# Kernel tuning notes

Hardware: AMD Instinct MI355X
Metric: run time of the kernel (lower is better)

Reference implementation:

```python
import jax, jax.numpy as jnp
import numpy as np

N = 50000      # nodes
E = 640000     # edges
F_IN = 128
F_OUT = 128


def setup_inputs() -> dict:
    key = jax.random.key(0)
    k1, k2, k3, k4, k5 = jax.random.split(key, 5)
    x = jax.random.normal(k1, (N, F_IN), jnp.float32)
    # binary observation mask (torch: mask.float())
    mask = (jax.random.uniform(k2, (N, F_IN)) < 0.5).astype(jnp.float32)
    edge_index = jax.random.randint(k3, (2, E), 0, N, dtype=jnp.int32)
    W = jax.random.normal(k4, (F_OUT, F_IN), jnp.float32) / np.sqrt(F_IN)
    b = jax.random.normal(k5, (F_OUT,), jnp.float32) * 0.01
    return {"x": x, "mask": mask, "edge_index": edge_index, "W": W, "b": b}


def reference(x, mask, edge_index, W, b):
    row, col = edge_index[0], edge_index[1]

    # --- get_symmetrically_normalized_adjacency: DAD = D^-1/2 A D^-1/2 ---
    ones_e = jnp.ones((edge_index.shape[1],), x.dtype)
    deg = jax.ops.segment_sum(ones_e, col, num_segments=N)
    dinv = jnp.where(deg > 0, deg ** -0.5, 0.0)  # inf -> 0
    w = dinv[row] * dinv[col]                    # [E] normalized edge weights

    def spmm(m):  # (adj @ m)[i] = sum_{e: row_e=i} w_e * m[col_e]
        return jax.ops.segment_sum(w[:, None] * m[col], row, num_segments=N)

    # x[x.isnan()] = 0
    x = jnp.nan_to_num(x)

    # adj @ ones_like(x) == rowsum(adj) broadcast over features
    rowsum = jax.ops.segment_sum(w, row, num_segments=N)  # [N]
    numerator = rowsum[:, None] * spmm(mask * x)          # [N, F_IN]
    denominator = spmm(mask)                              # [N, F_IN]
    ratio = jnp.nan_to_num(numerator / denominator)

    return ratio @ W.T + b
```

## Files before the change

kernel.cpp:

```cpp
#include <hip/hip_runtime.h>
#include <math.h>

#define NN 50000
#define NE 640000
#define F  128
#define NB 196
#define PACKB 12500
#define CHB 256
#define ECHUNK 2500
#define WPAD 136

typedef __attribute__((ext_vector_type(8))) short short8;
typedef __attribute__((ext_vector_type(4))) float floatx4;

__device__ inline unsigned f2bf_pk(float f0, float f1) {
    unsigned u0 = __float_as_uint(f0), u1 = __float_as_uint(f1);
    u0 = (u0 + 0x7fffu + ((u0 >> 16) & 1u)) >> 16;
    u1 = (u1 + 0x7fffu + ((u1 >> 16) & 1u)) >> 16;
    return (u1 << 16) | u0;
}

__device__ inline unsigned ilv4(unsigned a, unsigned b) {
    a = (a | (a << 2)) & 0x33u; a = (a | (a << 1)) & 0x55u;
    b = (b | (b << 2)) & 0x33u; b = (b | (b << 1)) & 0x55u;
    return a | (b << 1);
}

__global__ __launch_bounds__(256) void pc_kernel(const float* __restrict__ x,
                                                 const float* __restrict__ mask,
                                                 const int* __restrict__ row,
                                                 const int* __restrict__ col,
                                                 unsigned* __restrict__ mx,
                                                 unsigned char* __restrict__ rec,
                                                 int* __restrict__ crow,
                                                 int* __restrict__ ccol) {
    if (blockIdx.x < PACKB) {
        int lane = threadIdx.x & 63;
        int n = blockIdx.x * 4 + (threadIdx.x >> 6);
        float2 xv = ((const float2*)x)[(size_t)n * 64 + lane];
        float2 mv = ((const float2*)mask)[(size_t)n * 64 + lane];
        float x0 = (xv.x != xv.x) ? 0.f : xv.x;
        float x1 = (xv.y != xv.y) ? 0.f : xv.y;
        float p0 = (mv.x != 0.f) ? x0 : 0.f;
        float p1 = (mv.y != 0.f) ? x1 : 0.f;
        mx[(size_t)n * 64 + lane] = f2bf_pk(p0, p1);
        unsigned long long b0 = __ballot(mv.x != 0.f);
        unsigned long long b1 = __ballot(mv.y != 0.f);
        if (lane < 16) {
            unsigned nib0 = (unsigned)(b0 >> (4 * lane)) & 0xFu;
            unsigned nib1 = (unsigned)(b1 >> (4 * lane)) & 0xFu;
            rec[(size_t)n * 32 + lane] = (unsigned char)ilv4(nib0, nib1);
        }
    } else {
        __shared__ int hr[NB], hc[NB];
        for (int i = threadIdx.x; i < NB; i += 256) { hr[i] = 0; hc[i] = 0; }
        __syncthreads();
        int bid = blockIdx.x - PACKB;
        int e0 = bid * ECHUNK, e1 = e0 + ECHUNK;
        for (int e = e0 + threadIdx.x; e < e1; e += 256) {
            atomicAdd(&hr[row[e] >> 8], 1);
            atomicAdd(&hc[col[e] >> 8], 1);
        }
        __syncthreads();
        for (int i = threadIdx.x; i < NB; i += 256) {
            atomicAdd(&crow[i], hr[i]);
            atomicAdd(&ccol[i], hc[i]);
        }
    }
}

__global__ __launch_bounds__(256) void cscan_kernel(const int* __restrict__ crow,
                                                    const int* __restrict__ ccol,
                                                    int* __restrict__ crow_base,
                                                    int* __restrict__ ccol_base,
                                                    int* __restrict__ crow_cur,
                                                    int* __restrict__ ccol_cur,
                                                    int* __restrict__ rowstart) {
    __shared__ int ws[4];
    int t = threadIdx.x, lane = t & 63, wid = t >> 6;
    {
        int v = (t < NB) ? crow[t] : 0;
        int incl = v;
        #pragma unroll
        for (int off = 1; off < 64; off <<= 1) { int s = __shfl_up(incl, off); if (lane >= off) incl += s; }
        if (lane == 63) ws[wid] = incl;
        __syncthreads();
        int wbase = 0;
        for (int k = 0; k < wid; k++) wbase += ws[k];
        int ex = wbase + incl - v;
        if (t < NB) { crow_base[t] = ex; crow_cur[t] = ex; }
        if (t == 0) { crow_base[NB] = NE; rowstart[NN] = NE; }
        __syncthreads();
    }
    {
        int v = (t < NB) ? ccol[t] : 0;
        int incl = v;
        #pragma unroll
        for (int off = 1; off < 64; off <<= 1) { int s = __shfl_up(incl, off); if (lane >= off) incl += s; }
        if (lane == 63) ws[wid] = incl;
        __syncthreads();
        int wbase = 0;
        for (int k = 0; k < wid; k++) wbase += ws[k];
        int ex = wbase + incl - v;
        if (t < NB) { ccol_base[t] = ex; ccol_cur[t] = ex; }
        if (t == 0) ccol_base[NB] = NE;
    }
}

__global__ __launch_bounds__(256) void scatter_kernel(const int* __restrict__ row,
                                                      const int* __restrict__ col,
                                                      int* __restrict__ crow_cur,
                                                      int* __restrict__ ccol_cur,
                                                      unsigned* __restrict__ rrec,
                                                      unsigned char* __restrict__ crec) {
    __shared__ int cntR[NB], cntC[NB], curR[NB], curC[NB];
    for (int i = threadIdx.x; i < NB; i += 256) { cntR[i] = 0; cntC[i] = 0; }
    __syncthreads();
    int e0 = blockIdx.x * ECHUNK, e1 = e0 + ECHUNK;
    for (int e = e0 + threadIdx.x; e < e1; e += 256) {
        atomicAdd(&cntR[row[e] >> 8], 1);
        atomicAdd(&cntC[col[e] >> 8], 1);
    }
    __syncthreads();
    for (int i = threadIdx.x; i < NB; i += 256) {
        curR[i] = atomicAdd(&crow_cur[i], cntR[i]);
        curC[i] = atomicAdd(&ccol_cur[i], cntC[i]);
    }
    __syncthreads();
    for (int e = e0 + threadIdx.x; e < e1; e += 256) {
        int r = row[e], c = col[e];
        int pr = atomicAdd(&curR[r >> 8], 1);
        rrec[pr] = ((unsigned)(r & 255) << 16) | (unsigned)c;
        int pc = atomicAdd(&curC[c >> 8], 1);
        crec[pc] = (unsigned char)(c & 255);
    }
}

__global__ __launch_bounds__(256) void fine_kernel(const unsigned* __restrict__ rrec,
                                                   const unsigned char* __restrict__ crec,
                                                   const int* __restrict__ crow_base,
                                                   const int* __restrict__ ccol_base,
                                                   int* __restrict__ rowstart,
                                                   unsigned short* __restrict__ srcs,
                                                   unsigned char* __restrict__ rec) {
    __shared__ int hist[256];
    __shared__ int ws[4];
    int t = threadIdx.x, lane = t & 63, wid = t >> 6;
    hist[t] = 0;
    __syncthreads();
    if (blockIdx.x < NB) {
        int b = blockIdx.x;
        int s0 = crow_base[b], s1 = crow_base[b + 1];
        for (int j = s0 + t; j < s1; j += 256)
            atomicAdd(&hist[(rrec[j] >> 16) & 255], 1);
        __syncthreads();
        int v = hist[t];
        int incl = v;
        #pragma unroll
        for (int off = 1; off < 64; off <<= 1) { int s = __shfl_up(incl, off); if (lane >= off) incl += s; }
        if (lane == 63) ws[wid] = incl;
        __syncthreads();
        int wbase = 0;
        for (int k = 0; k < wid; k++) wbase += ws[k];
        int ex = wbase + incl - v;
        int node = b * 256 + t;
        if (node < NN) rowstart[node] = s0 + ex;
        hist[t] = ex;
        __syncthreads();
        for (int j = s0 + t; j < s1; j += 256) {
            unsigned r2 = rrec[j];
            int pos = atomicAdd(&hist[(r2 >> 16) & 255], 1);
            srcs[s0 + pos] = (unsigned short)(r2 & 0xFFFFu);
        }
    } else {
        int b = blockIdx.x - NB;
        int s0 = ccol_base[b], s1 = ccol_base[b + 1];
        for (int j = s0 + t; j < s1; j += 256)
            atomicAdd(&hist[crec[j]], 1);
        __syncthreads();
        int node = b * 256 + t;
        if (node < NN) {
            int d = hist[t];
            float dv = (d > 0) ? rsqrtf((float)d) : 0.0f;
            *(float*)(rec + (size_t)node * 32 + 16) = dv;
        }
    }
}

__global__ __launch_bounds__(256) void gather_kernel(
        const int* __restrict__ rowstart, const unsigned short* __restrict__ srcs,
        const uint4* __restrict__ mxv, const unsigned char* __restrict__ rec,
        unsigned* __restrict__ rb) {
    int lane = threadIdx.x & 63;
    int r = blockIdx.x * 4 + (threadIdx.x >> 6);
    int l16 = lane & 15, sub = lane >> 4;
    int s0 = rowstart[r], s1 = rowstart[r + 1];
    float dr = *(const float*)(rec + (size_t)r * 32 + 16);
    float num[8] = {0.f,0.f,0.f,0.f,0.f,0.f,0.f,0.f};
    float den[8] = {0.f,0.f,0.f,0.f,0.f,0.f,0.f,0.f};
    float S = 0.f;

    for (int j = s0; j < s1; j += 8) {
        {
            int jj = j + sub;
            int cl = (jj < s1) ? jj : (s1 - 1);
            int c = srcs[cl];
            float w = (jj < s1) ? *(const float*)(rec + (size_t)c * 32 + 16) : 0.f;
            uint4 u = mxv[(size_t)c * 16 + l16];
            unsigned mb = rec[(size_t)c * 32 + l16];
            float f[8];
            f[0] = __uint_as_float(u.x << 16); f[1] = __uint_as_float(u.x & 0xffff0000u);
            f[2] = __uint_as_float(u.y << 16); f[3] = __uint_as_float(u.y & 0xffff0000u);
            f[4] = __uint_as_float(u.z << 16); f[5] = __uint_as_float(u.z & 0xffff0000u);
            f[6] = __uint_as_float(u.w << 16); f[7] = __uint_as_float(u.w & 0xffff0000u);
            S += w;
            #pragma unroll
            for (int q = 0; q < 8; q++) {
                num[q] += w * f[q];
                den[q] += ((mb >> q) & 1u) ? w : 0.f;
            }
        }
        {
            int jj = j + 4 + sub;
            int cl = (jj < s1) ? jj : (s1 - 1);
            int c = srcs[cl];
            float w = (jj < s1) ? *(const float*)(rec + (size_t)c * 32 + 16) : 0.f;
            uint4 u = mxv[(size_t)c * 16 + l16];
            unsigned mb = rec[(size_t)c * 32 + l16];
            float f[8];
            f[0] = __uint_as_float(u.x << 16); f[1] = __uint_as_float(u.x & 0xffff0000u);
            f[2] = __uint_as_float(u.y << 16); f[3] = __uint_as_float(u.y & 0xffff0000u);
            f[4] = __uint_as_float(u.z << 16); f[5] = __uint_as_float(u.z & 0xffff0000u);
            f[6] = __uint_as_float(u.w << 16); f[7] = __uint_as_float(u.w & 0xffff0000u);
            S += w;
            #pragma unroll
            for (int q = 0; q < 8; q++) {
                num[q] += w * f[q];
                den[q] += ((mb >> q) & 1u) ? w : 0.f;
            }
        }
    }

    #pragma unroll
    for (int q = 0; q < 8; q++) {
        num[q] += __shfl_xor(num[q], 16); num[q] += __shfl_xor(num[q], 32);
        den[q] += __shfl_xor(den[q], 16); den[q] += __shfl_xor(den[q], 32);
    }
    S += __shfl_xor(S, 16); S += __shfl_xor(S, 32);

    if (sub == 0) {
        float kf = dr * S;
        float o[8];
        #pragma unroll
        for (int q = 0; q < 8; q++)
            o[q] = (den[q] != 0.f) ? kf * num[q] / den[q] : 0.f;
        uint4 pk;
        pk.x = f2bf_pk(o[0], o[1]);
        pk.y = f2bf_pk(o[2], o[3]);
        pk.z = f2bf_pk(o[4], o[5]);
        pk.w = f2bf_pk(o[6], o[7]);
        ((uint4*)rb)[(size_t)r * 16 + l16] = pk;
    }
}

__global__ __launch_bounds__(256) void gemm_kernel(const unsigned short* __restrict__ Ab,
                                                   const float* __restrict__ W,
                                                   const float* __restrict__ bias,
                                                   float* __restrict__ out) {
    __shared__ unsigned short Wlds[F * WPAD];
    int tid = threadIdx.x;

    for (int i = tid * 4; i < F * F; i += 256 * 4) {
        int c = i >> 7, k = i & 127;
        float4 v = *(const float4*)(W + i);
        unsigned lo = f2bf_pk(v.x, v.y);
        unsigned hi = f2bf_pk(v.z, v.w);
        *(uint2*)&Wlds[c * WPAD + k] = make_uint2(lo, hi);
    }
    __syncthreads();

    int lane = tid & 63, wid = tid >> 6;
    int m = lane & 15, quad = lane >> 4;
    int arow = blockIdx.x * 64 + wid * 16 + m;
    int lrow = (arow < NN) ? arow : (NN - 1);
    const unsigned short* Arow = Ab + (size_t)lrow * F + quad * 8;

    floatx4 acc[8];
    #pragma unroll
    for (int nt = 0; nt < 8; nt++) acc[nt] = (floatx4)(0.f);

    #pragma unroll
    for (int step = 0; step < 4; step++) {
        short8 af = *(const short8*)(Arow + step * 32);
        #pragma unroll
        for (int nt = 0; nt < 8; nt++) {
            short8 bf = *(const short8*)&Wlds[(nt * 16 + m) * WPAD + step * 32 + quad * 8];
            acc[nt] = __builtin_amdgcn_mfma_f32_16x16x32_bf16(af, bf, acc[nt], 0, 0, 0);
        }
    }

    int orow0 = blockIdx.x * 64 + wid * 16 + quad * 4;
    #pragma unroll
    for (int nt = 0; nt < 8; nt++) {
        float bv = bias[nt * 16 + m];
        #pragma unroll
        for (int p = 0; p < 4; p++) {
            int gr = orow0 + p;
            if (gr < NN) out[(size_t)gr * F + nt * 16 + m] = acc[nt][p] + bv;
        }
    }
}

extern "C" void kernel_launch(void* const* d_in, const int* in_sizes, int n_in,
                              void* d_out, int out_size, void* d_ws, size_t ws_size,
                              hipStream_t stream) {
    const float* x    = (const float*)d_in[0];
    const float* mask = (const float*)d_in[1];
    const int*   ei   = (const int*)d_in[2];
    const float* W    = (const float*)d_in[3];
    const float* b    = (const float*)d_in[4];
    float* out = (float*)d_out;

    const int* row = ei;
    const int* col = ei + NE;

    unsigned*       mx        = (unsigned*)d_ws;
    unsigned*       rb        = mx + (size_t)NN * 64;
    unsigned char*  rec       = (unsigned char*)(rb + (size_t)NN * 64);
    unsigned*       rrec      = (unsigned*)(rec + (size_t)NN * 32);
    unsigned short* srcs      = (unsigned short*)(rrec + NE);
    unsigned char*  crec      = (unsigned char*)(srcs + NE);
    int*            crow      = (int*)(crec + NE);
    int*            ccol      = crow + NB;
    int*            crow_base = ccol + NB;
    int*            ccol_base = crow_base + NB + 1;
    int*            crow_cur  = ccol_base + NB + 1;
    int*            ccol_cur  = crow_cur + NB;
    int*            rowstart  = ccol_cur + NB;

    hipMemsetAsync(crow, 0, 2 * NB * sizeof(int), stream);

    pc_kernel<<<PACKB + CHB, 256, 0, stream>>>(x, mask, row, col, mx, rec, crow, ccol);
    cscan_kernel<<<1, 256, 0, stream>>>(crow, ccol, crow_base, ccol_base,
                                        crow_cur, ccol_cur, rowstart);
    scatter_kernel<<<CHB, 256, 0, stream>>>(row, col, crow_cur, ccol_cur, rrec, crec);
    fine_kernel<<<2 * NB, 256, 0, stream>>>(rrec, crec, crow_base, ccol_base,
                                            rowstart, srcs, rec);
    gather_kernel<<<NN / 4, 256, 0, stream>>>(rowstart, srcs,
                                              (const uint4*)mx, rec, rb);
    gemm_kernel<<<(NN + 63) / 64, 256, 0, stream>>>((const unsigned short*)rb, W, b, out);
}
```

Measured before the change: 197.1 us.

## Pack bf16 edge weights with source index in padded CSR, drop gather bounds checks

Splits the fine CSR kernel into a column-degree pass and a row pass. The row pass now writes each edge as a 32-bit word holding the source index and the source's bf16 dinv weight, and pads each row by 8 zeroed slots so the gather loop runs without clamping or a second dinv lookup. The mask-bit record shrinks to 16 bytes per node, and the per-feature divide is replaced with a hardware reciprocal. The cost is an extra memset of the padded edge buffer, one more kernel launch, and bf16 rounding of edge weights, which loses some precision.

```diff
diff --git a/kernel.cpp b/kernel.cpp
--- a/kernel.cpp
+++ b/kernel.cpp
@@ -9,6 +9,7 @@
 #define CHB 256
 #define ECHUNK 2500
 #define WPAD 136
+#define SRCW_N (NE + 8 * NN)
 
 typedef __attribute__((ext_vector_type(8))) short short8;
 typedef __attribute__((ext_vector_type(4))) float floatx4;
@@ -49,7 +50,7 @@
         if (lane < 16) {
             unsigned nib0 = (unsigned)(b0 >> (4 * lane)) & 0xFu;
             unsigned nib1 = (unsigned)(b1 >> (4 * lane)) & 0xFu;
-            rec[(size_t)n * 32 + lane] = (unsigned char)ilv4(nib0, nib1);
+            rec[(size_t)n * 16 + lane] = (unsigned char)ilv4(nib0, nib1);
         }
     } else {
         __shared__ int hr[NB], hc[NB];
@@ -75,7 +76,7 @@
                                                     int* __restrict__ ccol_base,
                                                     int* __restrict__ crow_cur,
                                                     int* __restrict__ ccol_cur,
-                                                    int* __restrict__ rowstart) {
+                                                    int* __restrict__ rowstart_p) {
     __shared__ int ws[4];
     int t = threadIdx.x, lane = t & 63, wid = t >> 6;
     {
@@ -89,7 +90,7 @@
         for (int k = 0; k < wid; k++) wbase += ws[k];
         int ex = wbase + incl - v;
         if (t < NB) { crow_base[t] = ex; crow_cur[t] = ex; }
-        if (t == 0) { crow_base[NB] = NE; rowstart[NN] = NE; }
+        if (t == 0) { crow_base[NB] = NE; rowstart_p[NN] = NE + 8 * NN; }
         __syncthreads();
     }
     {
@@ -136,111 +137,106 @@
     }
 }
 
-__global__ __launch_bounds__(256) void fine_kernel(const unsigned* __restrict__ rrec,
-                                                   const unsigned char* __restrict__ crec,
-                                                   const int* __restrict__ crow_base,
-                                                   const int* __restrict__ ccol_base,
-                                                   int* __restrict__ rowstart,
-                                                   unsigned short* __restrict__ srcs,
-                                                   unsigned char* __restrict__ rec) {
+__global__ __launch_bounds__(256) void finecol_kernel(const unsigned char* __restrict__ crec,
+                                                      const int* __restrict__ ccol_base,
+                                                      float* __restrict__ dinv) {
+    __shared__ int hist[256];
+    int b = blockIdx.x;
+    int s0 = ccol_base[b], s1 = ccol_base[b + 1];
+    int t = threadIdx.x;
+    hist[t] = 0;
+    __syncthreads();
+    for (int j = s0 + t; j < s1; j += 256)
+        atomicAdd(&hist[crec[j]], 1);
+    __syncthreads();
+    int node = b * 256 + t;
+    if (node < NN) {
+        int d = hist[t];
+        dinv[node] = (d > 0) ? rsqrtf((float)d) : 0.0f;
+    }
+}
+
+__global__ __launch_bounds__(256) void finerow_kernel(const unsigned* __restrict__ rrec,
+                                                      const int* __restrict__ crow_base,
+                                                      const float* __restrict__ dinv,
+                                                      int* __restrict__ rowstart_p,
+                                                      unsigned* __restrict__ srcs_w) {
     __shared__ int hist[256];
     __shared__ int ws[4];
+    int b = blockIdx.x;
+    int s0 = crow_base[b], s1 = crow_base[b + 1];
     int t = threadIdx.x, lane = t & 63, wid = t >> 6;
     hist[t] = 0;
     __syncthreads();
-    if (blockIdx.x < NB) {
-        int b = blockIdx.x;
-        int s0 = crow_base[b], s1 = crow_base[b + 1];
-        for (int j = s0 + t; j < s1; j += 256)
-            atomicAdd(&hist[(rrec[j] >> 16) & 255], 1);
-        __syncthreads();
-        int v = hist[t];
-        int incl = v;
-        #pragma unroll
-        for (int off = 1; off < 64; off <<= 1) { int s = __shfl_up(incl, off); if (lane >= off) incl += s; }
-        if (lane == 63) ws[wid] = incl;
-        __syncthreads();
-        int wbase = 0;
-        for (int k = 0; k < wid; k++) wbase += ws[k];
-        int ex = wbase + incl - v;
-        int node = b * 256 + t;
-        if (node < NN) rowstart[node] = s0 + ex;
-        hist[t] = ex;
-        __syncthreads();
-        for (int j = s0 + t; j < s1; j += 256) {
-            unsigned r2 = rrec[j];
-            int pos = atomicAdd(&hist[(r2 >> 16) & 255], 1);
-            srcs[s0 + pos] = (unsigned short)(r2 & 0xFFFFu);
-        }
-    } else {
-        int b = blockIdx.x - NB;
-        int s0 = ccol_base[b], s1 = ccol_base[b + 1];
-        for (int j = s0 + t; j < s1; j += 256)
-            atomicAdd(&hist[crec[j]], 1);
-        __syncthreads();
-        int node = b * 256 + t;
-        if (node < NN) {
-            int d = hist[t];
-            float dv = (d > 0) ? rsqrtf((float)d) : 0.0f;
-            *(float*)(rec + (size_t)node * 32 + 16) = dv;
-        }
+    for (int j = s0 + t; j < s1; j += 256)
+        atomicAdd(&hist[(rrec[j] >> 16) & 255], 1);
+    __syncthreads();
+    int v = hist[t];
+    int incl = v;
+    #pragma unroll
+    for (int off = 1; off < 64; off <<= 1) { int s = __shfl_up(incl, off); if (lane >= off) incl += s; }
+    if (lane == 63) ws[wid] = incl;
+    __syncthreads();
+    int wbase = 0;
+    for (int k = 0; k < wid; k++) wbase += ws[k];
+    int ex = wbase + incl - v;
+    int pbase = s0 + 2048 * b;
+    int node = b * 256 + t;
+    if (node < NN) rowstart_p[node] = pbase + ex + 8 * t;
+    hist[t] = ex + 8 * t;
+    __syncthreads();
+    for (int j = s0 + t; j < s1; j += 256) {
+        unsigned r2 = rrec[j];
+        int c = r2 & 0xFFFF;
+        int pos = atomicAdd(&hist[(r2 >> 16) & 255], 1);
+        srcs_w[pbase + pos] = f2bf_pk(0.f, dinv[c]) | (unsigned)c;
     }
 }
 
 __global__ __launch_bounds__(256) void gather_kernel(
-        const int* __restrict__ rowstart, const unsigned short* __restrict__ srcs,
+        const int* __restrict__ rowstart_p, const unsigned* __restrict__ srcs_w,
+        const float* __restrict__ dinv,
         const uint4* __restrict__ mxv, const unsigned char* __restrict__ rec,
         unsigned* __restrict__ rb) {
     int lane = threadIdx.x & 63;
     int r = blockIdx.x * 4 + (threadIdx.x >> 6);
     int l16 = lane & 15, sub = lane >> 4;
-    int s0 = rowstart[r], s1 = rowstart[r + 1];
-    float dr = *(const float*)(rec + (size_t)r * 32 + 16);
-    float num[8] = {0.f,0.f,0.f,0.f,0.f,0.f,0.f,0.f};
-    float den[8] = {0.f,0.f,0.f,0.f,0.f,0.f,0.f,0.f};
+    int s0p = rowstart_p[r];
+    int L = rowstart_p[r + 1] - s0p - 8;
+    float dr = dinv[r];
+    floatx4 n0 = (floatx4)(0.f), n1 = (floatx4)(0.f);
+    floatx4 d0 = (floatx4)(0.f), d1 = (floatx4)(0.f);
     float S = 0.f;
 
-    for (int j = s0; j < s1; j += 8) {
-        {
-            int jj = j + sub;
-            int cl = (jj < s1) ? jj : (s1 - 1);
-            int c = srcs[cl];
-            float w = (jj < s1) ? *(const float*)(rec + (size_t)c * 32 + 16) : 0.f;
-            uint4 u = mxv[(size_t)c * 16 + l16];
-            unsigned mb = rec[(size_t)c * 32 + l16];
-            float f[8];
-            f[0] = __uint_as_float(u.x << 16); f[1] = __uint_as_float(u.x & 0xffff0000u);
-            f[2] = __uint_as_float(u.y << 16); f[3] = __uint_as_float(u.y & 0xffff0000u);
-            f[4] = __uint_as_float(u.z << 16); f[5] = __uint_as_float(u.z & 0xffff0000u);
-            f[6] = __uint_as_float(u.w << 16); f[7] = __uint_as_float(u.w & 0xffff0000u);
+    for (int j = 0; j < L; j += 8) {
+        #pragma unroll
+        for (int g = 0; g < 2; g++) {
+            unsigned u = srcs_w[s0p + j + 4 * g + sub];
+            int c = u & 0xFFFFu;
+            float w = __uint_as_float(u & 0xFFFF0000u);
+            uint4 m4 = mxv[c * 16 + l16];
+            unsigned mb = rec[c * 16 + l16];
+            floatx4 fa, fb;
+            fa.x = __uint_as_float(m4.x << 16); fa.y = __uint_as_float(m4.x & 0xffff0000u);
+            fa.z = __uint_as_float(m4.y << 16); fa.w = __uint_as_float(m4.y & 0xffff0000u);
+            fb.x = __uint_as_float(m4.z << 16); fb.y = __uint_as_float(m4.z & 0xffff0000u);
+            fb.z = __uint_as_float(m4.w << 16); fb.w = __uint_as_float(m4.w & 0xffff0000u);
+            n0 += w * fa;
+            n1 += w * fb;
+            d0.x += ((mb >> 0) & 1u) ? w : 0.f;
+            d0.y += ((mb >> 1) & 1u) ? w : 0.f;
+            d0.z += ((mb >> 2) & 1u) ? w : 0.f;
+            d0.w += ((mb >> 3) & 1u) ? w : 0.f;
+            d1.x += ((mb >> 4) & 1u) ? w : 0.f;
+            d1.y += ((mb >> 5) & 1u) ? w : 0.f;
+            d1.z += ((mb >> 6) & 1u) ? w : 0.f;
+            d1.w += ((mb >> 7) & 1u) ? w : 0.f;
             S += w;
-            #pragma unroll
-            for (int q = 0; q < 8; q++) {
-                num[q] += w * f[q];
-                den[q] += ((mb >> q) & 1u) ? w : 0.f;
-            }
-        }
-        {
-            int jj = j + 4 + sub;
-            int cl = (jj < s1) ? jj : (s1 - 1);
-            int c = srcs[cl];
-            float w = (jj < s1) ? *(const float*)(rec + (size_t)c * 32 + 16) : 0.f;
-            uint4 u = mxv[(size_t)c * 16 + l16];
-            unsigned mb = rec[(size_t)c * 32 + l16];
-            float f[8];
-            f[0] = __uint_as_float(u.x << 16); f[1] = __uint_as_float(u.x & 0xffff0000u);
-            f[2] = __uint_as_float(u.y << 16); f[3] = __uint_as_float(u.y & 0xffff0000u);
-            f[4] = __uint_as_float(u.z << 16); f[5] = __uint_as_float(u.z & 0xffff0000u);
-            f[6] = __uint_as_float(u.w << 16); f[7] = __uint_as_float(u.w & 0xffff0000u);
-            S += w;
-            #pragma unroll
-            for (int q = 0; q < 8; q++) {
-                num[q] += w * f[q];
-                den[q] += ((mb >> q) & 1u) ? w : 0.f;
-            }
-        }
-    }
-
+        }
+    }
+
+    float num[8] = {n0.x, n0.y, n0.z, n0.w, n1.x, n1.y, n1.z, n1.w};
+    float den[8] = {d0.x, d0.y, d0.z, d0.w, d1.x, d1.y, d1.z, d1.w};
     #pragma unroll
     for (int q = 0; q < 8; q++) {
         num[q] += __shfl_xor(num[q], 16); num[q] += __shfl_xor(num[q], 32);
@@ -253,7 +249,7 @@
         float o[8];
         #pragma unroll
         for (int q = 0; q < 8; q++)
-            o[q] = (den[q] != 0.f) ? kf * num[q] / den[q] : 0.f;
+            o[q] = (den[q] != 0.f) ? kf * num[q] * __builtin_amdgcn_rcpf(den[q]) : 0.f;
         uint4 pk;
         pk.x = f2bf_pk(o[0], o[1]);
         pk.y = f2bf_pk(o[2], o[3]);
@@ -326,27 +322,29 @@
 
     unsigned*       mx        = (unsigned*)d_ws;
     unsigned*       rb        = mx + (size_t)NN * 64;
-    unsigned char*  rec       = (unsigned char*)(rb + (size_t)NN * 64);
-    unsigned*       rrec      = (unsigned*)(rec + (size_t)NN * 32);
-    unsigned short* srcs      = (unsigned short*)(rrec + NE);
-    unsigned char*  crec      = (unsigned char*)(srcs + NE);
-    int*            crow      = (int*)(crec + NE);
+    unsigned*       srcs_w    = rb + (size_t)NN * 64;
+    unsigned*       rrec      = srcs_w + SRCW_N;
+    unsigned char*  rec       = (unsigned char*)(rrec + NE);
+    unsigned char*  crec      = rec + (size_t)NN * 16;
+    float*          dinv      = (float*)(crec + NE);
+    int*            crow      = (int*)(dinv + NN);
     int*            ccol      = crow + NB;
     int*            crow_base = ccol + NB;
     int*            ccol_base = crow_base + NB + 1;
     int*            crow_cur  = ccol_base + NB + 1;
     int*            ccol_cur  = crow_cur + NB;
-    int*            rowstart  = ccol_cur + NB;
+    int*            rowstart_p= ccol_cur + NB;
 
     hipMemsetAsync(crow, 0, 2 * NB * sizeof(int), stream);
+    hipMemsetAsync(srcs_w, 0, (size_t)SRCW_N * sizeof(unsigned), stream);
 
     pc_kernel<<<PACKB + CHB, 256, 0, stream>>>(x, mask, row, col, mx, rec, crow, ccol);
     cscan_kernel<<<1, 256, 0, stream>>>(crow, ccol, crow_base, ccol_base,
-                                        crow_cur, ccol_cur, rowstart);
+                                        crow_cur, ccol_cur, rowstart_p);
     scatter_kernel<<<CHB, 256, 0, stream>>>(row, col, crow_cur, ccol_cur, rrec, crec);
-    fine_kernel<<<2 * NB, 256, 0, stream>>>(rrec, crec, crow_base, ccol_base,
-                                            rowstart, srcs, rec);
-    gather_kernel<<<NN / 4, 256, 0, stream>>>(rowstart, srcs,
+    finecol_kernel<<<NB, 256, 0, stream>>>(crec, ccol_base, dinv);
+    finerow_kernel<<<NB, 256, 0, stream>>>(rrec, crow_base, dinv, rowstart_p, srcs_w);
+    gather_kernel<<<NN / 4, 256, 0, stream>>>(rowstart_p, srcs_w, dinv,
                                               (const uint4*)mx, rec, rb);
     gemm_kernel<<<(NN + 63) / 64, 256, 0, stream>>>((const unsigned short*)rb, W, b, out);
 }
```

Measured after the change: 202.6 us. 2.8% more time.
